# Optimization experiments

Hardware: AMD Instinct MI355X
Metric: run time of the kernel (lower is better)

Reference implementation:

```python
import jax, jax.numpy as jnp
import numpy as np

DIM = 768
HEADS = 12
HEAD_DIM = DIM // HEADS
SCALE = HEAD_DIM ** -0.5


def setup_inputs() -> dict:
    key = jax.random.key(0)
    ks = jax.random.split(key, 9)
    B, N, M, C = 4, 1024, 1024, DIM
    std = C ** -0.5
    return {
        "q": jax.random.normal(ks[0], (B, N, C), jnp.float32),
        "k": jax.random.normal(ks[1], (B, M, C), jnp.float32),
        "v": jax.random.normal(ks[2], (B, M, C), jnp.float32),
        "mask": jax.random.uniform(ks[3], (B, N, M), jnp.float32),
        "Wq": jax.random.normal(ks[4], (C, C), jnp.float32) * std,
        "Wk": jax.random.normal(ks[5], (C, C), jnp.float32) * std,
        "Wv": jax.random.normal(ks[6], (C, C), jnp.float32) * std,
        "Wp": jax.random.normal(ks[7], (C, C), jnp.float32) * std,
        "bp": jax.random.normal(ks[8], (C,), jnp.float32) * 0.01,
    }


def reference(q, k, v, mask, Wq, Wk, Wv, Wp, bp):
    B, N, C = q.shape
    M = k.shape[1]
    H, D = HEADS, HEAD_DIM
    qh = (q @ Wq).reshape(B, N, H, D)
    kh = (k @ Wk).reshape(B, M, H, D)
    vh = (v @ Wv).reshape(B, M, H, D)
    attn = jnp.einsum('bnhd,bmhd->bhnm', qh, kh) * SCALE
    attn = jax.nn.softmax(attn, axis=-1)
    # post-softmax multiplicative mask, broadcast over heads
    attn = attn * mask[:, None, :, :]
    x = jnp.einsum('bhnm,bmhd->bnhd', attn, vh).reshape(B, N, C)
    return x @ Wp + bp
```

## Files before the change

kernel.cpp:

```cpp
#include <hip/hip_runtime.h>

typedef __bf16 bf16x8 __attribute__((ext_vector_type(8)));
typedef float f32x4 __attribute__((ext_vector_type(4)));

__device__ __forceinline__ unsigned short f2bf(float f) {
  union { float f; unsigned u; } x; x.f = f;
  unsigned r = x.u + 0x7FFFu + ((x.u >> 16) & 1u);
  return (unsigned short)(r >> 16);
}

__device__ __forceinline__ float fast_exp2(float x) {
  float r;
  asm("v_exp_f32 %0, %1" : "=v"(r) : "v"(x));
  return r;
}

__device__ __forceinline__ void gload_lds16(const void* g, void* l) {
  __builtin_amdgcn_global_load_lds(
      (const __attribute__((address_space(1))) unsigned int*)g,
      (__attribute__((address_space(3))) unsigned int*)l, 16, 0, 0);
}

__device__ __forceinline__ f32x4 mfma16(bf16x8 a, bf16x8 b, f32x4 c) {
  return __builtin_amdgcn_mfma_f32_16x16x32_bf16(a, b, c, 0, 0, 0);
}

__device__ __forceinline__ bf16x8 pack8(const f32x4& a, const f32x4& b) {
  bf16x8 r;
  r[0] = (__bf16)a[0]; r[1] = (__bf16)a[1]; r[2] = (__bf16)a[2]; r[3] = (__bf16)a[3];
  r[4] = (__bf16)b[0]; r[5] = (__bf16)b[1]; r[6] = (__bf16)b[2]; r[7] = (__bf16)b[3];
  return r;
}

__global__ __launch_bounds__(256) void conv_qkv(const float* __restrict__ q,
                                                const float* __restrict__ k,
                                                const float* __restrict__ v,
                                                unsigned short* __restrict__ dst) {
  const float* src = (blockIdx.y == 0) ? q : (blockIdx.y == 1 ? k : v);
  size_t i = ((size_t)blockIdx.x * 256 + threadIdx.x) * 4;
  float4 f = *(const float4*)(src + i);
  ushort4 u;
  u.x = f2bf(f.x); u.y = f2bf(f.y); u.z = f2bf(f.z); u.w = f2bf(f.w);
  *(ushort4*)(dst + (size_t)blockIdx.y * (4096u * 768u) + i) = u;
}

__global__ __launch_bounds__(256) void conv_w(const float* __restrict__ W0,
                                              const float* __restrict__ W1,
                                              const float* __restrict__ W2,
                                              const float* __restrict__ W3,
                                              unsigned short* __restrict__ Wt) {
  __shared__ float tile[32][33];
  const float* W = (blockIdx.z == 0) ? W0 : (blockIdx.z == 1) ? W1
                   : (blockIdx.z == 2) ? W2 : W3;
  int tx = threadIdx.x, ty = threadIdx.y;
  int n0 = blockIdx.x * 32, k0 = blockIdx.y * 32;
#pragma unroll
  for (int i = 0; i < 4; ++i)
    tile[ty * 4 + i][tx] = W[(size_t)(k0 + ty * 4 + i) * 768 + n0 + tx];
  __syncthreads();
  unsigned short* o = Wt + (size_t)blockIdx.z * 768 * 768;
#pragma unroll
  for (int i = 0; i < 4; ++i)
    o[(size_t)(n0 + ty * 4 + i) * 768 + k0 + tx] = f2bf(tile[tx][ty * 4 + i]);
}

__global__ __launch_bounds__(256) void gemm_qkv(const unsigned short* __restrict__ Abase,
                                                const unsigned short* __restrict__ Wt,
                                                unsigned short* __restrict__ Hq,
                                                unsigned short* __restrict__ Hk,
                                                unsigned short* __restrict__ Hvt) {
  __shared__ unsigned short As[2][128 * 64], Bs[2][128 * 64];
  const int flat = blockIdx.x;
  const int lid = (flat & 7) * 72 + (flat >> 3);
  const int z = lid / 192;
  const int rem = lid - z * 192;
  const int m0 = (rem & 31) * 128;
  const int n0 = (rem >> 5) * 128;
  const unsigned short* A = Abase + (size_t)z * 4096 * 768;
  const unsigned short* B = Wt + (size_t)z * 768 * 768;
  const int t = threadIdx.x, l = t & 63, wid = t >> 6;
  const int g = l >> 4, c16 = l & 15;
  const int wm = (wid >> 1) * 64, wn = (wid & 1) * 64;

  auto stage = [&](unsigned short* dst, const unsigned short* src, int base, int k0) {
#pragma unroll
    for (int i = 0; i < 4; ++i) {
      int fc = i * 256 + t, r = fc >> 3, c = (fc & 7) ^ ((r >> 1) & 7);
      gload_lds16(src + (size_t)(base + r) * 768 + k0 + c * 8, (char*)dst + fc * 16);
    }
  };
  stage(As[0], A, m0, 0);
  stage(Bs[0], B, n0, 0);
  asm volatile("s_waitcnt vmcnt(0)" ::: "memory");
  __syncthreads();
  f32x4 acc[4][4] = {};
  for (int s = 0; s < 12; ++s) {
    const int cur = s & 1;
    if (s < 11) {
      stage(As[cur ^ 1], A, m0, (s + 1) * 64);
      stage(Bs[cur ^ 1], B, n0, (s + 1) * 64);
    }
#pragma unroll
    for (int kk = 0; kk < 2; ++kk) {
      const int ch = kk * 4 + g;
      bf16x8 a[4], bw[4];
#pragma unroll
      for (int mi = 0; mi < 4; ++mi) {
        int r = wm + mi * 16 + c16;
        a[mi] = *(const bf16x8*)((char*)As[cur] + r * 128 + (((ch ^ (r >> 1)) & 7) << 4));
      }
#pragma unroll
      for (int ni = 0; ni < 4; ++ni) {
        int r = wn + ni * 16 + c16;
        bw[ni] = *(const bf16x8*)((char*)Bs[cur] + r * 128 + (((ch ^ (r >> 1)) & 7) << 4));
      }
#pragma unroll
      for (int mi = 0; mi < 4; ++mi)
#pragma unroll
        for (int ni = 0; ni < 4; ++ni)
          acc[mi][ni] = mfma16(a[mi], bw[ni], acc[mi][ni]);
    }
    __syncthreads();
  }

  if (z < 2) {
    const float f = (z == 0) ? 0.125f * 1.44269504088896341f : 1.0f;
    unsigned short* C = (z == 0) ? Hq : Hk;
#pragma unroll
    for (int mi = 0; mi < 4; ++mi)
#pragma unroll
      for (int ni = 0; ni < 4; ++ni) {
        int col = n0 + wn + ni * 16 + c16;
        int row = m0 + wm + mi * 16 + g * 4;
#pragma unroll
        for (int j = 0; j < 4; ++j)
          C[(size_t)(row + j) * 768 + col] = f2bf(acc[mi][ni][j] * f);
      }
  } else {
#pragma unroll
    for (int mi = 0; mi < 4; ++mi) {
      int rowbase = m0 + wm + mi * 16;
      int bat = rowbase >> 10;
      int mloc = (rowbase & 1023) + g * 4;
#pragma unroll
      for (int ni = 0; ni < 4; ++ni) {
        int col = n0 + wn + ni * 16 + c16;
        ushort4 u;
        u.x = f2bf(acc[mi][ni][0]); u.y = f2bf(acc[mi][ni][1]);
        u.z = f2bf(acc[mi][ni][2]); u.w = f2bf(acc[mi][ni][3]);
        *(ushort4*)(Hvt + (((size_t)(bat * 768 + col)) << 10) + mloc) = u;
      }
    }
  }
}

__global__ __launch_bounds__(256) void attn(const unsigned short* __restrict__ qh,
                                            const unsigned short* __restrict__ kh,
                                            const unsigned short* __restrict__ vhT,
                                            const float* __restrict__ mask,
                                            unsigned short* __restrict__ xb) {
  __shared__ unsigned short Ks[3][64 * 64], Vts[3][64 * 64];
  const int flat = blockIdx.x;
  const int lid = (flat & 7) * 96 + (flat >> 3);
  const int h = lid % 12, qt = (lid / 12) & 15, b = lid / 192;
  const int t = threadIdx.x, l = t & 63, wid = t >> 6;
  const int g = l >> 4, c16 = l & 15;

  const unsigned short* qp =
      qh + ((size_t)(b * 1024 + qt * 64 + wid * 16 + c16)) * 768 + h * 64 + g * 8;
  bf16x8 aq0 = *(const bf16x8*)qp;
  bf16x8 aq1 = *(const bf16x8*)(qp + 32);

  const int fc0 = t, r0 = fc0 >> 3, c0 = (fc0 & 7) ^ ((r0 >> 1) & 7);
  const int fc1 = 256 + t, r1 = fc1 >> 3, c1 = (fc1 & 7) ^ ((r1 >> 1) & 7);
  const int s0 = 32 * (r0 >> 5) + 8 * ((r0 >> 2) & 3) + 4 * ((r0 >> 4) & 1) + (r0 & 3);
  const int s1 = 32 * (r1 >> 5) + 8 * ((r1 >> 2) & 3) + 4 * ((r1 >> 4) & 1) + (r1 & 3);
  const unsigned short* kp0 = kh + (size_t)(b * 1024 + s0) * 768 + h * 64 + c0 * 8;
  const unsigned short* kp1 = kh + (size_t)(b * 1024 + s1) * 768 + h * 64 + c1 * 8;
  const unsigned short* vp0 = vhT + ((size_t)(b * 768 + h * 64 + r0)) * 1024 + c0 * 8;
  const unsigned short* vp1 = vhT + ((size_t)(b * 768 + h * 64 + r1)) * 1024 + c1 * 8;

  auto stageKV = [&](int buf) {
    char* kd = (char*)Ks[buf];
    char* vd = (char*)Vts[buf];
    gload_lds16(kp0, kd + fc0 * 16);
    gload_lds16(kp1, kd + fc1 * 16);
    gload_lds16(vp0, vd + fc0 * 16);
    gload_lds16(vp1, vd + fc1 * 16);
    kp0 += 64 * 768; kp1 += 64 * 768; vp0 += 64; vp1 += 64;
  };

  const float* mq = mask + ((size_t)(b * 1024 + qt * 64 + wid * 16 + c16)) * 1024 + 8 * g;

  stageKV(0);
  stageKV(1);
  asm volatile("s_waitcnt vmcnt(4)" ::: "memory");
  __builtin_amdgcn_s_barrier();

  f32x4 o[4] = {};
  f32x4 ls = {0.f, 0.f, 0.f, 0.f};

  for (int kv = 0; kv < 16; ++kv) {
    const int cur = kv % 3;
    if (kv < 14) stageKV((kv + 2) % 3);
    const float* mk = mq + kv * 64;
    f32x4 mreg[4];
    mreg[0] = *(const f32x4*)(mk);
    mreg[1] = *(const f32x4*)(mk + 4);
    mreg[2] = *(const f32x4*)(mk + 32);
    mreg[3] = *(const f32x4*)(mk + 36);
    f32x4 p[4] = {};
#pragma unroll
    for (int kk = 0; kk < 2; ++kk) {
      const int ch = kk * 4 + g;
      bf16x8 aq = kk ? aq1 : aq0;
#pragma unroll
      for (int ni = 0; ni < 4; ++ni) {
        int r = ni * 16 + c16;
        bf16x8 bk = *(const bf16x8*)((char*)Ks[cur] + r * 128 + (((ch ^ (r >> 1)) & 7) << 4));
        p[ni] = mfma16(bk, aq, p[ni]);
      }
    }
#pragma unroll
    for (int ni = 0; ni < 4; ++ni) {
      float e0 = fast_exp2(p[ni][0]);
      float e1 = fast_exp2(p[ni][1]);
      float e2 = fast_exp2(p[ni][2]);
      float e3 = fast_exp2(p[ni][3]);
      ls[ni] += (e0 + e1) + (e2 + e3);
      p[ni][0] = e0 * mreg[ni][0];
      p[ni][1] = e1 * mreg[ni][1];
      p[ni][2] = e2 * mreg[ni][2];
      p[ni][3] = e3 * mreg[ni][3];
    }
    bf16x8 pa0 = pack8(p[0], p[1]);
    bf16x8 pa1 = pack8(p[2], p[3]);
#pragma unroll
    for (int kk = 0; kk < 2; ++kk) {
      const int ch = kk * 4 + g;
      bf16x8 ap = kk ? pa1 : pa0;
#pragma unroll
      for (int ni = 0; ni < 4; ++ni) {
        int r = ni * 16 + c16;
        bf16x8 bv = *(const bf16x8*)((char*)Vts[cur] + r * 128 + (((ch ^ (r >> 1)) & 7) << 4));
        o[ni] = mfma16(ap, bv, o[ni]);
      }
    }
    if (kv < 14) {
      asm volatile("s_waitcnt vmcnt(4)" ::: "memory");
      __builtin_amdgcn_s_barrier();
    } else if (kv == 14) {
      asm volatile("s_waitcnt vmcnt(0)" ::: "memory");
      __builtin_amdgcn_s_barrier();
    }
  }
  float s = (ls[0] + ls[1]) + (ls[2] + ls[3]);
  s += __shfl_xor(s, 16);
  s += __shfl_xor(s, 32);
  float rinv = 1.0f / s;
  const int rb = (l & 48) | ((l >> 2) & 12);
  float rj[4];
#pragma unroll
  for (int j = 0; j < 4; ++j) rj[j] = __shfl(rinv, rb + j);
#pragma unroll
  for (int ni = 0; ni < 4; ++ni) {
    int col = h * 64 + ni * 16 + c16;
    int row = qt * 64 + wid * 16 + g * 4;
#pragma unroll
    for (int j = 0; j < 4; ++j)
      xb[((size_t)(b * 1024) + row + j) * 768 + col] = f2bf(o[ni][j] * rj[j]);
  }
}

__global__ __launch_bounds__(256) void gemm_proj(const unsigned short* __restrict__ A,
                                                 const unsigned short* __restrict__ B,
                                                 const float* __restrict__ bias,
                                                 float* __restrict__ C) {
  __shared__ unsigned short As[2][64 * 64], Bs[2][64 * 64];
  const int flat = blockIdx.x;
  const int lid = (flat & 7) * 96 + (flat >> 3);
  const int m0 = (lid & 63) * 64;
  const int n0 = (lid >> 6) * 64;
  const int t = threadIdx.x, l = t & 63, wid = t >> 6;
  const int g = l >> 4, c16 = l & 15;
  const int wm = (wid >> 1) * 32, wn = (wid & 1) * 32;
  auto stage = [&](unsigned short* dst, const unsigned short* src, int base, int k0) {
#pragma unroll
    for (int i = 0; i < 2; ++i) {
      int fc = i * 256 + t, r = fc >> 3, c = (fc & 7) ^ ((r >> 1) & 7);
      gload_lds16(src + (size_t)(base + r) * 768 + k0 + c * 8, (char*)dst + fc * 16);
    }
  };
  stage(As[0], A, m0, 0);
  stage(Bs[0], B, n0, 0);
  asm volatile("s_waitcnt vmcnt(0)" ::: "memory");
  __syncthreads();
  f32x4 acc[2][2] = {};
  for (int s = 0; s < 12; ++s) {
    const int cur = s & 1;
    if (s < 11) {
      stage(As[cur ^ 1], A, m0, (s + 1) * 64);
      stage(Bs[cur ^ 1], B, n0, (s + 1) * 64);
    }
#pragma unroll
    for (int kk = 0; kk < 2; ++kk) {
      const int ch = kk * 4 + g;
      bf16x8 a[2], bw[2];
#pragma unroll
      for (int mi = 0; mi < 2; ++mi) {
        int r = wm + mi * 16 + c16;
        a[mi] = *(const bf16x8*)((char*)As[cur] + r * 128 + (((ch ^ (r >> 1)) & 7) << 4));
      }
#pragma unroll
      for (int ni = 0; ni < 2; ++ni) {
        int r = wn + ni * 16 + c16;
        bw[ni] = *(const bf16x8*)((char*)Bs[cur] + r * 128 + (((ch ^ (r >> 1)) & 7) << 4));
      }
#pragma unroll
      for (int mi = 0; mi < 2; ++mi)
#pragma unroll
        for (int ni = 0; ni < 2; ++ni)
          acc[mi][ni] = mfma16(a[mi], bw[ni], acc[mi][ni]);
    }
    __syncthreads();
  }
#pragma unroll
  for (int mi = 0; mi < 2; ++mi)
#pragma unroll
    for (int ni = 0; ni < 2; ++ni) {
      int col = n0 + wn + ni * 16 + c16;
      int row = m0 + wm + mi * 16 + g * 4;
      float bv = bias[col];
#pragma unroll
      for (int j = 0; j < 4; ++j)
        C[(size_t)(row + j) * 768 + col] = acc[mi][ni][j] + bv;
    }
}

extern "C" void kernel_launch(void* const* d_in, const int* in_sizes, int n_in,
                              void* d_out, int out_size, void* d_ws, size_t ws_size,
                              hipStream_t stream) {
  const float* q    = (const float*)d_in[0];
  const float* k    = (const float*)d_in[1];
  const float* v    = (const float*)d_in[2];
  const float* mask = (const float*)d_in[3];
  const float* Wq   = (const float*)d_in[4];
  const float* Wk   = (const float*)d_in[5];
  const float* Wv   = (const float*)d_in[6];
  const float* Wp   = (const float*)d_in[7];
  const float* bp   = (const float*)d_in[8];
  float* out = (float*)d_out;

  const size_t MN = (size_t)4096 * 768;
  const size_t WW = (size_t)768 * 768;
  unsigned short* qkv_bf = (unsigned short*)d_ws;
  unsigned short* wt     = qkv_bf + 3 * MN;
  unsigned short* heads  = wt + 4 * WW;
  unsigned short* xb     = heads + 3 * MN;

  conv_qkv<<<dim3(3072, 3), 256, 0, stream>>>(q, k, v, qkv_bf);
  conv_w<<<dim3(24, 24, 4), dim3(32, 8), 0, stream>>>(Wq, Wk, Wv, Wp, wt);
  gemm_qkv<<<dim3(576), 256, 0, stream>>>(qkv_bf, wt, heads, heads + MN, heads + 2 * MN);
  attn<<<dim3(768), 256, 0, stream>>>(heads, heads + MN, heads + 2 * MN, mask, xb);
  gemm_proj<<<dim3(768), 256, 0, stream>>>(xb, wt + 3 * WW, bp, out);
}
```

Before: 94.18 us.

## Merge conversion kernels and widen attention KV tile to 128 with double buffering

The two fp32-to-bf16 conversion kernels become one launch, with the weight-transpose blocks mapped onto a fourth grid row, which saves a kernel launch. The attention kernel now processes 128 keys per iteration with two LDS buffers instead of 64 keys with three buffers. This halves the number of loop iterations and barriers and issues larger loads per stage. The cost is a shallower prefetch depth, a full vmcnt(0) wait via __syncthreads each iteration, and more registers for the doubled score and mask arrays. The K and V swizzle layouts are reworked to match, and the conv_all grid launches 3072 weight blocks of which 768 exit immediately.

```diff
diff --git a/kernel.cpp b/kernel.cpp
--- a/kernel.cpp
+++ b/kernel.cpp
@@ -32,36 +32,39 @@
   return r;
 }
 
-__global__ __launch_bounds__(256) void conv_qkv(const float* __restrict__ q,
+__global__ __launch_bounds__(256) void conv_all(const float* __restrict__ q,
                                                 const float* __restrict__ k,
                                                 const float* __restrict__ v,
-                                                unsigned short* __restrict__ dst) {
-  const float* src = (blockIdx.y == 0) ? q : (blockIdx.y == 1 ? k : v);
-  size_t i = ((size_t)blockIdx.x * 256 + threadIdx.x) * 4;
-  float4 f = *(const float4*)(src + i);
-  ushort4 u;
-  u.x = f2bf(f.x); u.y = f2bf(f.y); u.z = f2bf(f.z); u.w = f2bf(f.w);
-  *(ushort4*)(dst + (size_t)blockIdx.y * (4096u * 768u) + i) = u;
-}
-
-__global__ __launch_bounds__(256) void conv_w(const float* __restrict__ W0,
-                                              const float* __restrict__ W1,
-                                              const float* __restrict__ W2,
-                                              const float* __restrict__ W3,
-                                              unsigned short* __restrict__ Wt) {
+                                                const float* __restrict__ W0,
+                                                const float* __restrict__ W1,
+                                                const float* __restrict__ W2,
+                                                const float* __restrict__ W3,
+                                                unsigned short* __restrict__ dst,
+                                                unsigned short* __restrict__ Wt) {
   __shared__ float tile[32][33];
-  const float* W = (blockIdx.z == 0) ? W0 : (blockIdx.z == 1) ? W1
-                   : (blockIdx.z == 2) ? W2 : W3;
-  int tx = threadIdx.x, ty = threadIdx.y;
-  int n0 = blockIdx.x * 32, k0 = blockIdx.y * 32;
-#pragma unroll
-  for (int i = 0; i < 4; ++i)
-    tile[ty * 4 + i][tx] = W[(size_t)(k0 + ty * 4 + i) * 768 + n0 + tx];
-  __syncthreads();
-  unsigned short* o = Wt + (size_t)blockIdx.z * 768 * 768;
-#pragma unroll
-  for (int i = 0; i < 4; ++i)
-    o[(size_t)(n0 + ty * 4 + i) * 768 + k0 + tx] = f2bf(tile[tx][ty * 4 + i]);
+  if (blockIdx.y < 3) {
+    const float* src = (blockIdx.y == 0) ? q : (blockIdx.y == 1 ? k : v);
+    size_t i = ((size_t)blockIdx.x * 256 + threadIdx.x) * 4;
+    float4 f = *(const float4*)(src + i);
+    ushort4 u;
+    u.x = f2bf(f.x); u.y = f2bf(f.y); u.z = f2bf(f.z); u.w = f2bf(f.w);
+    *(ushort4*)(dst + (size_t)blockIdx.y * (4096u * 768u) + i) = u;
+  } else {
+    if (blockIdx.x >= 2304) return;
+    int idx = blockIdx.x;
+    int bx = idx % 24, by = (idx / 24) % 24, bz = idx / 576;
+    const float* W = (bz == 0) ? W0 : (bz == 1) ? W1 : (bz == 2) ? W2 : W3;
+    int tx = threadIdx.x & 31, ty = threadIdx.x >> 5;
+    int n0 = bx * 32, k0 = by * 32;
+#pragma unroll
+    for (int i = 0; i < 4; ++i)
+      tile[ty * 4 + i][tx] = W[(size_t)(k0 + ty * 4 + i) * 768 + n0 + tx];
+    __syncthreads();
+    unsigned short* o = Wt + (size_t)bz * 768 * 768;
+#pragma unroll
+    for (int i = 0; i < 4; ++i)
+      o[(size_t)(n0 + ty * 4 + i) * 768 + k0 + tx] = f2bf(tile[tx][ty * 4 + i]);
+  }
 }
 
 __global__ __launch_bounds__(256) void gemm_qkv(const unsigned short* __restrict__ Abase,
@@ -159,7 +162,7 @@
                                             const unsigned short* __restrict__ vhT,
                                             const float* __restrict__ mask,
                                             unsigned short* __restrict__ xb) {
-  __shared__ unsigned short Ks[3][64 * 64], Vts[3][64 * 64];
+  __shared__ unsigned short Ks[2][128 * 64], Vts[2][64 * 128];
   const int flat = blockIdx.x;
   const int lid = (flat & 7) * 96 + (flat >> 3);
   const int h = lid % 12, qt = (lid / 12) & 15, b = lid / 192;
@@ -171,63 +174,70 @@
   bf16x8 aq0 = *(const bf16x8*)qp;
   bf16x8 aq1 = *(const bf16x8*)(qp + 32);
 
-  const int fc0 = t, r0 = fc0 >> 3, c0 = (fc0 & 7) ^ ((r0 >> 1) & 7);
-  const int fc1 = 256 + t, r1 = fc1 >> 3, c1 = (fc1 & 7) ^ ((r1 >> 1) & 7);
-  const int s0 = 32 * (r0 >> 5) + 8 * ((r0 >> 2) & 3) + 4 * ((r0 >> 4) & 1) + (r0 & 3);
-  const int s1 = 32 * (r1 >> 5) + 8 * ((r1 >> 2) & 3) + 4 * ((r1 >> 4) & 1) + (r1 & 3);
-  const unsigned short* kp0 = kh + (size_t)(b * 1024 + s0) * 768 + h * 64 + c0 * 8;
-  const unsigned short* kp1 = kh + (size_t)(b * 1024 + s1) * 768 + h * 64 + c1 * 8;
-  const unsigned short* vp0 = vhT + ((size_t)(b * 768 + h * 64 + r0)) * 1024 + c0 * 8;
-  const unsigned short* vp1 = vhT + ((size_t)(b * 768 + h * 64 + r1)) * 1024 + c1 * 8;
+  const int r0 = t >> 3;
+  const int kc = (t & 7) ^ ((r0 >> 1) & 7);
+  const int sig0 = 8 * ((r0 >> 2) & 3) + 4 * ((r0 >> 4) & 1) + (r0 & 3);
+  const unsigned short* kp = kh + (size_t)(b * 1024 + sig0) * 768 + h * 64 + kc * 8;
+  const int vr0 = t >> 4;
+  const int vcA = (t & 15) ^ (vr0 >> 1);
+  const unsigned short* vpA = vhT + ((size_t)(b * 768 + h * 64 + vr0)) * 1024 + vcA * 8;
+  const unsigned short* vpB = vhT + ((size_t)(b * 768 + h * 64 + vr0)) * 1024 + (vcA ^ 8) * 8;
 
   auto stageKV = [&](int buf) {
     char* kd = (char*)Ks[buf];
     char* vd = (char*)Vts[buf];
-    gload_lds16(kp0, kd + fc0 * 16);
-    gload_lds16(kp1, kd + fc1 * 16);
-    gload_lds16(vp0, vd + fc0 * 16);
-    gload_lds16(vp1, vd + fc1 * 16);
-    kp0 += 64 * 768; kp1 += 64 * 768; vp0 += 64; vp1 += 64;
+    gload_lds16(kp,            kd + t * 16);
+    gload_lds16(kp + 32 * 768, kd + (256 + t) * 16);
+    gload_lds16(kp + 64 * 768, kd + (512 + t) * 16);
+    gload_lds16(kp + 96 * 768, kd + (768 + t) * 16);
+    gload_lds16(vpA,             vd + t * 16);
+    gload_lds16(vpB + 16 * 1024, vd + (256 + t) * 16);
+    gload_lds16(vpA + 32 * 1024, vd + (512 + t) * 16);
+    gload_lds16(vpB + 48 * 1024, vd + (768 + t) * 16);
+    kp += 128 * 768; vpA += 128; vpB += 128;
   };
 
   const float* mq = mask + ((size_t)(b * 1024 + qt * 64 + wid * 16 + c16)) * 1024 + 8 * g;
 
   stageKV(0);
-  stageKV(1);
-  asm volatile("s_waitcnt vmcnt(4)" ::: "memory");
+  asm volatile("s_waitcnt vmcnt(0)" ::: "memory");
   __builtin_amdgcn_s_barrier();
 
   f32x4 o[4] = {};
   f32x4 ls = {0.f, 0.f, 0.f, 0.f};
 
-  for (int kv = 0; kv < 16; ++kv) {
-    const int cur = kv % 3;
-    if (kv < 14) stageKV((kv + 2) % 3);
-    const float* mk = mq + kv * 64;
-    f32x4 mreg[4];
+  for (int kv = 0; kv < 8; ++kv) {
+    const int cur = kv & 1;
+    if (kv < 7) stageKV(cur ^ 1);
+    const float* mk = mq + kv * 128;
+    f32x4 mreg[8];
     mreg[0] = *(const f32x4*)(mk);
     mreg[1] = *(const f32x4*)(mk + 4);
     mreg[2] = *(const f32x4*)(mk + 32);
     mreg[3] = *(const f32x4*)(mk + 36);
-    f32x4 p[4] = {};
+    mreg[4] = *(const f32x4*)(mk + 64);
+    mreg[5] = *(const f32x4*)(mk + 68);
+    mreg[6] = *(const f32x4*)(mk + 96);
+    mreg[7] = *(const f32x4*)(mk + 100);
+    f32x4 p[8] = {};
 #pragma unroll
     for (int kk = 0; kk < 2; ++kk) {
       const int ch = kk * 4 + g;
       bf16x8 aq = kk ? aq1 : aq0;
 #pragma unroll
-      for (int ni = 0; ni < 4; ++ni) {
+      for (int ni = 0; ni < 8; ++ni) {
         int r = ni * 16 + c16;
-        bf16x8 bk = *(const bf16x8*)((char*)Ks[cur] + r * 128 + (((ch ^ (r >> 1)) & 7) << 4));
+        bf16x8 bk = *(const bf16x8*)((char*)Ks[cur] + r * 128 + (((ch ^ (c16 >> 1)) & 7) << 4));
         p[ni] = mfma16(bk, aq, p[ni]);
       }
     }
 #pragma unroll
-    for (int ni = 0; ni < 4; ++ni) {
+    for (int ni = 0; ni < 8; ++ni) {
       float e0 = fast_exp2(p[ni][0]);
       float e1 = fast_exp2(p[ni][1]);
       float e2 = fast_exp2(p[ni][2]);
       float e3 = fast_exp2(p[ni][3]);
-      ls[ni] += (e0 + e1) + (e2 + e3);
+      ls[ni & 3] += (e0 + e1) + (e2 + e3);
       p[ni][0] = e0 * mreg[ni][0];
       p[ni][1] = e1 * mreg[ni][1];
       p[ni][2] = e2 * mreg[ni][2];
@@ -235,25 +245,23 @@
     }
     bf16x8 pa0 = pack8(p[0], p[1]);
     bf16x8 pa1 = pack8(p[2], p[3]);
-#pragma unroll
-    for (int kk = 0; kk < 2; ++kk) {
+    bf16x8 pa2 = pack8(p[4], p[5]);
+    bf16x8 pa3 = pack8(p[6], p[7]);
+#pragma unroll
+    for (int kk = 0; kk < 4; ++kk) {
       const int ch = kk * 4 + g;
-      bf16x8 ap = kk ? pa1 : pa0;
+      bf16x8 ap = (kk == 0) ? pa0 : (kk == 1) ? pa1 : (kk == 2) ? pa2 : pa3;
 #pragma unroll
       for (int ni = 0; ni < 4; ++ni) {
         int r = ni * 16 + c16;
-        bf16x8 bv = *(const bf16x8*)((char*)Vts[cur] + r * 128 + (((ch ^ (r >> 1)) & 7) << 4));
+        bf16x8 bv = *(const bf16x8*)((char*)Vts[cur] + r * 256 +
+                                     (((ch ^ ((ni & 1) * 8 + (c16 >> 1))) & 15) << 4));
         o[ni] = mfma16(ap, bv, o[ni]);
       }
     }
-    if (kv < 14) {
-      asm volatile("s_waitcnt vmcnt(4)" ::: "memory");
-      __builtin_amdgcn_s_barrier();
-    } else if (kv == 14) {
-      asm volatile("s_waitcnt vmcnt(0)" ::: "memory");
-      __builtin_amdgcn_s_barrier();
-    }
-  }
+    if (kv < 7) __syncthreads();
+  }
+
   float s = (ls[0] + ls[1]) + (ls[2] + ls[3]);
   s += __shfl_xor(s, 16);
   s += __shfl_xor(s, 32);
@@ -358,8 +366,7 @@
   unsigned short* heads  = wt + 4 * WW;
   unsigned short* xb     = heads + 3 * MN;
 
-  conv_qkv<<<dim3(3072, 3), 256, 0, stream>>>(q, k, v, qkv_bf);
-  conv_w<<<dim3(24, 24, 4), dim3(32, 8), 0, stream>>>(Wq, Wk, Wv, Wp, wt);
+  conv_all<<<dim3(3072, 4), 256, 0, stream>>>(q, k, v, Wq, Wk, Wv, Wp, qkv_bf, wt);
   gemm_qkv<<<dim3(576), 256, 0, stream>>>(qkv_bf, wt, heads, heads + MN, heads + 2 * MN);
   attn<<<dim3(768), 256, 0, stream>>>(heads, heads + MN, heads + 2 * MN, mask, xb);
   gemm_proj<<<dim3(768), 256, 0, stream>>>(xb, wt + 3 * WW, bp, out);
```

New measurement: 107.9 us. 14.6% more time.

## Fuse fp32-to-bf16 input conversion into QKV GEMM A-tile loading

Applied to the files above, without the earlier changes.

Removes the separate conv_qkv kernel. The QKV GEMM now loads fp32 q/k/v rows into registers, converts them to bf16, and writes them into swizzled LDS after the MFMA work of each stage, while B still streams in through direct global-to-LDS loads. This saves one kernel launch plus a bf16 write and re-read of roughly 19 MB of activations, in exchange for twice the global read bytes for A inside the GEMM and higher register pressure. The conv_w launch also switches to a 1D block layout.

```diff
diff --git a/kernel.cpp b/kernel.cpp
--- a/kernel.cpp
+++ b/kernel.cpp
@@ -30,18 +30,6 @@
   r[0] = (__bf16)a[0]; r[1] = (__bf16)a[1]; r[2] = (__bf16)a[2]; r[3] = (__bf16)a[3];
   r[4] = (__bf16)b[0]; r[5] = (__bf16)b[1]; r[6] = (__bf16)b[2]; r[7] = (__bf16)b[3];
   return r;
-}
-
-__global__ __launch_bounds__(256) void conv_qkv(const float* __restrict__ q,
-                                                const float* __restrict__ k,
-                                                const float* __restrict__ v,
-                                                unsigned short* __restrict__ dst) {
-  const float* src = (blockIdx.y == 0) ? q : (blockIdx.y == 1 ? k : v);
-  size_t i = ((size_t)blockIdx.x * 256 + threadIdx.x) * 4;
-  float4 f = *(const float4*)(src + i);
-  ushort4 u;
-  u.x = f2bf(f.x); u.y = f2bf(f.y); u.z = f2bf(f.z); u.w = f2bf(f.w);
-  *(ushort4*)(dst + (size_t)blockIdx.y * (4096u * 768u) + i) = u;
 }
 
 __global__ __launch_bounds__(256) void conv_w(const float* __restrict__ W0,
@@ -52,7 +40,7 @@
   __shared__ float tile[32][33];
   const float* W = (blockIdx.z == 0) ? W0 : (blockIdx.z == 1) ? W1
                    : (blockIdx.z == 2) ? W2 : W3;
-  int tx = threadIdx.x, ty = threadIdx.y;
+  int tx = threadIdx.x & 31, ty = threadIdx.x >> 5;
   int n0 = blockIdx.x * 32, k0 = blockIdx.y * 32;
 #pragma unroll
   for (int i = 0; i < 4; ++i)
@@ -64,7 +52,9 @@
     o[(size_t)(n0 + ty * 4 + i) * 768 + k0 + tx] = f2bf(tile[tx][ty * 4 + i]);
 }
 
-__global__ __launch_bounds__(256) void gemm_qkv(const unsigned short* __restrict__ Abase,
+__global__ __launch_bounds__(256) void gemm_qkv(const float* __restrict__ qf,
+                                                const float* __restrict__ kf,
+                                                const float* __restrict__ vf,
                                                 const unsigned short* __restrict__ Wt,
                                                 unsigned short* __restrict__ Hq,
                                                 unsigned short* __restrict__ Hk,
@@ -76,29 +66,49 @@
   const int rem = lid - z * 192;
   const int m0 = (rem & 31) * 128;
   const int n0 = (rem >> 5) * 128;
-  const unsigned short* A = Abase + (size_t)z * 4096 * 768;
+  const float* A = (z == 0) ? qf : (z == 1) ? kf : vf;
   const unsigned short* B = Wt + (size_t)z * 768 * 768;
   const int t = threadIdx.x, l = t & 63, wid = t >> 6;
   const int g = l >> 4, c16 = l & 15;
   const int wm = (wid >> 1) * 64, wn = (wid & 1) * 64;
 
-  auto stage = [&](unsigned short* dst, const unsigned short* src, int base, int k0) {
+  const int rA = t >> 1, cA = (t & 1) * 32;
+  f32x4 fA[8];
+  auto loadA = [&](int k0) {
+    const float* a = A + (size_t)(m0 + rA) * 768 + k0 + cA;
+#pragma unroll
+    for (int i = 0; i < 8; ++i) fA[i] = *(const f32x4*)(a + i * 4);
+  };
+  auto writeA = [&](unsigned short* dst) {
+    const int cb = (t & 1) * 4;
+#pragma unroll
+    for (int c = 0; c < 4; ++c) {
+      bf16x8 w;
+#pragma unroll
+      for (int j = 0; j < 8; ++j) w[j] = (__bf16)fA[c * 2 + (j >> 2)][j & 3];
+      *(bf16x8*)((char*)dst + rA * 128 + ((((cb + c) ^ (rA >> 1)) & 7) << 4)) = w;
+    }
+  };
+  auto stageB = [&](unsigned short* dst, int k0) {
 #pragma unroll
     for (int i = 0; i < 4; ++i) {
       int fc = i * 256 + t, r = fc >> 3, c = (fc & 7) ^ ((r >> 1) & 7);
-      gload_lds16(src + (size_t)(base + r) * 768 + k0 + c * 8, (char*)dst + fc * 16);
-    }
-  };
-  stage(As[0], A, m0, 0);
-  stage(Bs[0], B, n0, 0);
-  asm volatile("s_waitcnt vmcnt(0)" ::: "memory");
+      gload_lds16(B + (size_t)(n0 + r) * 768 + k0 + c * 8, (char*)dst + fc * 16);
+    }
+  };
+
+  loadA(0);
+  stageB(Bs[0], 0);
+  asm volatile("s_waitcnt vmcnt(4)" ::: "memory");
+  writeA(As[0]);
   __syncthreads();
+
   f32x4 acc[4][4] = {};
   for (int s = 0; s < 12; ++s) {
     const int cur = s & 1;
     if (s < 11) {
-      stage(As[cur ^ 1], A, m0, (s + 1) * 64);
-      stage(Bs[cur ^ 1], B, n0, (s + 1) * 64);
+      loadA((s + 1) * 64);
+      stageB(Bs[cur ^ 1], (s + 1) * 64);
     }
 #pragma unroll
     for (int kk = 0; kk < 2; ++kk) {
@@ -119,6 +129,10 @@
 #pragma unroll
         for (int ni = 0; ni < 4; ++ni)
           acc[mi][ni] = mfma16(a[mi], bw[ni], acc[mi][ni]);
+    }
+    if (s < 11) {
+      asm volatile("s_waitcnt vmcnt(4)" ::: "memory");
+      writeA(As[cur ^ 1]);
     }
     __syncthreads();
   }
@@ -353,14 +367,12 @@
 
   const size_t MN = (size_t)4096 * 768;
   const size_t WW = (size_t)768 * 768;
-  unsigned short* qkv_bf = (unsigned short*)d_ws;
-  unsigned short* wt     = qkv_bf + 3 * MN;
-  unsigned short* heads  = wt + 4 * WW;
-  unsigned short* xb     = heads + 3 * MN;
-
-  conv_qkv<<<dim3(3072, 3), 256, 0, stream>>>(q, k, v, qkv_bf);
-  conv_w<<<dim3(24, 24, 4), dim3(32, 8), 0, stream>>>(Wq, Wk, Wv, Wp, wt);
-  gemm_qkv<<<dim3(576), 256, 0, stream>>>(qkv_bf, wt, heads, heads + MN, heads + 2 * MN);
+  unsigned short* wt    = (unsigned short*)d_ws;
+  unsigned short* heads = wt + 4 * WW;
+  unsigned short* xb    = heads + 3 * MN;
+
+  conv_w<<<dim3(24, 24, 4), 256, 0, stream>>>(Wq, Wk, Wv, Wp, wt);
+  gemm_qkv<<<dim3(576), 256, 0, stream>>>(q, k, v, wt, heads, heads + MN, heads + 2 * MN);
   attn<<<dim3(768), 256, 0, stream>>>(heads, heads + MN, heads + 2 * MN, mask, xb);
   gemm_proj<<<dim3(768), 256, 0, stream>>>(xb, wt + 3 * WW, bp, out);
 }
```

New measurement: 118.8 us. 26.2% more time.
